# Kernel tuning notes

Hardware: AMD Instinct MI355X
Metric: run time of the kernel (lower is better)

Reference implementation:

```python
import jax, jax.numpy as jnp
import numpy as np
from jax import lax

B = 32        # true batch size (groups)
C_IN = 64     # per-sample input channels
C_OUT = 64    # per-sample output channels
H = W = 256
KH = KW = 3


def setup_inputs() -> dict:
    key = jax.random.key(0)
    kx, kk = jax.random.split(key)
    # x folds the batch into channels: [1, B*C_in, H, W]
    x = jax.random.normal(kx, (1, B * C_IN, H, W), dtype=jnp.float32)
    # per-sample kernels stacked along output-filter axis: [B*C_out, C_in, kH, kW]
    kernels = jax.random.normal(kk, (B * C_OUT, C_IN, KH, KW), dtype=jnp.float32)
    return {"x": x, "kernels": kernels, "batch_size": B}


def reference(x, kernels, batch_size):
    # F.conv2d(x, kernels, stride=1, padding='same', groups=batch_size)
    # Grouped conv with feature_group_count = batch_size (one group per sample).
    out = lax.conv_general_dilated(
        x,
        kernels,
        window_strides=(1, 1),
        padding="SAME",
        feature_group_count=batch_size,
        dimension_numbers=("NCHW", "OIHW", "NCHW"),
    )
    return out
```

## Files before the change

kernel.cpp:

```cpp
#include <hip/hip_runtime.h>
#include <hip/hip_bf16.h>


typedef __bf16 bf16x8 __attribute__((ext_vector_type(8)));
typedef float  f32x4  __attribute__((ext_vector_type(4)));

#define NB 32
#define NH 256
#define NW 256
#define TILE_H 4
#define TILE_W 64
#define XROWS 6
#define XCOLS 68
#define HWSZ ((size_t)NH * NW)

template<int P> struct IC { static constexpr int v = P; };

__device__ __forceinline__ void gload16(const float* g, float* lds) {
    __builtin_amdgcn_global_load_lds(
        (const __attribute__((address_space(1))) unsigned int*)g,
        (__attribute__((address_space(3))) unsigned int*)lds, 16, 0, 0);
}

__global__ void repack_weights_kernel(const float* __restrict__ wsrc,
                                      __bf16* __restrict__ pk) {
    int t = blockIdx.x * blockDim.x + threadIdx.x;
    if (t >= NB * 9 * 4 * 2 * 64) return;
    int lane = t & 63;
    int r = t >> 6;
    int kc = r & 1;  r >>= 1;
    int mt = r & 3;  r >>= 2;
    int tap = r % 9;
    int b   = r / 9;
    int co  = b * 64 + mt * 16 + (lane & 15);
    int ci0 = kc * 32 + (lane >> 4) * 8;
    bf16x8 v;
#pragma unroll
    for (int j = 0; j < 8; ++j) {
        v[j] = (__bf16)wsrc[(co * 64 + ci0 + j) * 9 + tap];
    }
    *reinterpret_cast<bf16x8*>(pk + (size_t)t * 8) = v;
}

__launch_bounds__(256)
__global__ void conv_mfma_kernel(const float* __restrict__ x,
                                 const __bf16* __restrict__ pk,
                                 float* __restrict__ out) {
    __shared__ __align__(16) __bf16 xs[XROWS * XCOLS * 32];
    __shared__ __align__(16) float  scratch[XROWS * 32 * 64];

    const int orig = blockIdx.x;
    const int wg   = (orig & 7) * 1024 + (orig >> 3);
    const int b    = wg >> 8;
    const int by   = (wg >> 2) & 63;
    const int bx   = wg & 3;
    const int h0   = by * TILE_H;
    const int w0   = bx * TILE_W;

    const int tid  = threadIdx.x;
    const int wid  = tid >> 6;
    const int lane = tid & 63;
    const int nl   = lane & 15;
    const int kgrp = lane >> 4;

    const __bf16* pkb = pk + (size_t)b * 9 * 4096;

    bf16x8 af[4][4];
    auto load_af = [&](int g) {
        const int tap = (g >= 9) ? g - 9 : g;
        const int kc  = (g >= 9) ? 1 : 0;
        const int sl  = g & 3;
#pragma unroll
        for (int mt = 0; mt < 4; ++mt)
            af[sl][mt] = *reinterpret_cast<const bf16x8*>(
                pkb + tap * 4096 + ((mt * 2 + kc) * 64 + lane) * 8);
    };

    f32x4 acc[4][4];
#pragma unroll
    for (int mt = 0; mt < 4; ++mt)
#pragma unroll
        for (int q = 0; q < 4; ++q)
            acc[mt][q] = (f32x4){0.f, 0.f, 0.f, 0.f};

    const int hside = tid & 1;
    const int hidx  = tid >> 1;
    const int hrr   = hidx % 6;
    const int hoo   = hidx / 6;
    const int hch   = hside ? 65 : 0;
    const int hwv   = hside ? (w0 + 64) : (w0 - 1);
    float hreg[8];
    bool  hz = false;

    auto issue_gload = [&](int kcv) {
#pragma unroll
        for (int m = 0; m < 12; ++m) {
            const int I  = wid * 12 + m;
            const int r  = I >> 3;
            const int cb = I & 7;
            const int hh = h0 - 1 + r;
            const int hc = min(max(hh, 0), NH - 1);
            const float* src = x
                + ((size_t)(b * 64 + kcv * 32 + cb * 4 + (lane >> 4)) * NH + hc) * NW
                + w0 + (lane & 15) * 4;
            gload16(src, scratch + (r * 32 + cb * 4) * 64);
        }
    };

    auto issue_halo = [&](int kcv) {
        if (tid < 48) {
            const int hh = h0 - 1 + hrr;
            hz = (hwv < 0) || (hwv > NW - 1) || (hh < 0) || (hh > NH - 1);
            const int wc2 = min(max(hwv, 0), NW - 1);
            const int hc2 = min(max(hh, 0), NH - 1);
            const float* s = x + ((size_t)(b * 64 + kcv * 32 + hoo * 8) * NH + hc2) * NW + wc2;
#pragma unroll
            for (int j = 0; j < 8; ++j) hreg[j] = s[j * HWSZ];
        }
    };

    auto cvt = [&]() {
#pragma unroll
        for (int rr = 0; rr < XROWS; ++rr) {
            const int hh = h0 - 1 + rr;
            const bool z = (hh < 0) || (hh > NH - 1);
            float v[8];
#pragma unroll
            for (int j = 0; j < 8; ++j)
                v[j] = scratch[(rr * 32 + wid * 8 + j) * 64 + lane];
            bf16x8 o8;
#pragma unroll
            for (int j = 0; j < 8; ++j) o8[j] = z ? (__bf16)0.f : (__bf16)v[j];
            const int c = lane + 1;
            *reinterpret_cast<bf16x8*>(
                xs + (rr * XCOLS + c) * 32 + ((wid ^ ((c >> 1) & 3)) * 8)) = o8;
        }
        if (tid < 48) {
            bf16x8 o8;
#pragma unroll
            for (int j = 0; j < 8; ++j) o8[j] = hz ? (__bf16)0.f : (__bf16)hreg[j];
            *reinterpret_cast<bf16x8*>(xs + (hrr * XCOLS + hch) * 32 + hoo * 8) = o8;
        }
    };

    auto comp = [&](auto parc, auto issc) {
        constexpr int PAR = decltype(parc)::v;
        constexpr int ISS = decltype(issc)::v;
#pragma unroll
        for (int tap = 0; tap < 9; ++tap) {
            const int g = PAR * 9 + tap;
            if (g + 2 < 18) load_af(g + 2);
            if constexpr (ISS) {
                if (tap == 3) { issue_gload(1); issue_halo(1); }
            }
            const int kh = tap / 3;
            const int kw = tap - kh * 3;
            const int rowbase = (wid + kh) * XCOLS;
            const int fs = g & 3;
#pragma unroll
            for (int q = 0; q < 4; ++q) {
                const int cc   = q * 16 + nl + kw;
                const int slot = (cc >> 1) & 3;
                bf16x8 bfv = *reinterpret_cast<const bf16x8*>(
                    xs + (rowbase + cc) * 32 + ((kgrp ^ slot) * 8));
#pragma unroll
                for (int mt = 0; mt < 4; ++mt)
                    acc[mt][q] = __builtin_amdgcn_mfma_f32_16x16x32_bf16(
                        af[fs][mt], bfv, acc[mt][q], 0, 0, 0);
            }
        }
    };

    load_af(0);
    load_af(1);
    issue_gload(0);
    issue_halo(0);
    __syncthreads();
    cvt();
    __syncthreads();
    comp(IC<0>{}, IC<1>{});
    __syncthreads();
    cvt();
    __syncthreads();
    comp(IC<1>{}, IC<0>{});

    const int mrow = kgrp * 4;
    const int h = h0 + wid;
#pragma unroll
    for (int mt = 0; mt < 4; ++mt) {
#pragma unroll
        for (int q = 0; q < 4; ++q) {
            const int ww = w0 + q * 16 + nl;
#pragma unroll
            for (int rg = 0; rg < 4; ++rg) {
                const int co = mt * 16 + mrow + rg;
                out[((size_t)(b * 64 + co) * NH + h) * NW + ww] = acc[mt][q][rg];
            }
        }
    }
}

extern "C" void kernel_launch(void* const* d_in, const int* in_sizes, int n_in,
                              void* d_out, int out_size, void* d_ws, size_t ws_size,
                              hipStream_t stream) {
    const float* x = (const float*)d_in[0];
    const float* w = (const float*)d_in[1];
    float* out = (float*)d_out;
    __bf16* pk = (__bf16*)d_ws;

    {
        int total = NB * 9 * 4 * 2 * 64;
        int blk = 256;
        int grid = (total + blk - 1) / blk;
        hipLaunchKernelGGL(repack_weights_kernel, dim3(grid), dim3(blk), 0, stream,
                           w, pk);
    }
    {
        dim3 grid(8192);
        hipLaunchKernelGGL(conv_mfma_kernel, grid, dim3(256), 0, stream,
                           x, pk, out);
    }
}
```

Measured before the change: 323.8 us.

## Split output channels across 8 waves and load halo via async LDS loads

Doubles the workgroup to 512 threads (8 waves), with each wave computing half of the 64 output channels for one row. All 9 taps of weights are preloaded per channel half instead of rotating 4 slots. The halo columns now go through global_load_lds into a small shared buffer rather than per-thread register loads, and the unused LDS padding shrinks from 68 to 66 columns. This raises the wave count per block to improve latency hiding, at the cost of more registers for the preloaded weights and duplicate B-fragment LDS reads across the two channel-halves.

```diff
diff --git a/kernel.cpp b/kernel.cpp
--- a/kernel.cpp
+++ b/kernel.cpp
@@ -11,7 +11,7 @@
 #define TILE_H 4
 #define TILE_W 64
 #define XROWS 6
-#define XCOLS 68
+#define XCOLS 66
 #define HWSZ ((size_t)NH * NW)
 
 template<int P> struct IC { static constexpr int v = P; };
@@ -20,6 +20,11 @@
     __builtin_amdgcn_global_load_lds(
         (const __attribute__((address_space(1))) unsigned int*)g,
         (__attribute__((address_space(3))) unsigned int*)lds, 16, 0, 0);
+}
+__device__ __forceinline__ void gload4(const float* g, float* lds) {
+    __builtin_amdgcn_global_load_lds(
+        (const __attribute__((address_space(1))) unsigned int*)g,
+        (__attribute__((address_space(3))) unsigned int*)lds, 4, 0, 0);
 }
 
 __global__ void repack_weights_kernel(const float* __restrict__ wsrc,
@@ -42,12 +47,13 @@
     *reinterpret_cast<bf16x8*>(pk + (size_t)t * 8) = v;
 }
 
-__launch_bounds__(256)
+__launch_bounds__(512, 4)
 __global__ void conv_mfma_kernel(const float* __restrict__ x,
                                  const __bf16* __restrict__ pk,
                                  float* __restrict__ out) {
     __shared__ __align__(16) __bf16 xs[XROWS * XCOLS * 32];
     __shared__ __align__(16) float  scratch[XROWS * 32 * 64];
+    __shared__ __align__(16) float  shalo[2 * XROWS * 32];
 
     const int orig = blockIdx.x;
     const int wg   = (orig & 7) * 1024 + (orig >> 3);
@@ -62,40 +68,33 @@
     const int lane = tid & 63;
     const int nl   = lane & 15;
     const int kgrp = lane >> 4;
+    const int rloc = wid >> 1;
+    const int ch   = wid & 1;
 
     const __bf16* pkb = pk + (size_t)b * 9 * 4096;
 
-    bf16x8 af[4][4];
-    auto load_af = [&](int g) {
-        const int tap = (g >= 9) ? g - 9 : g;
-        const int kc  = (g >= 9) ? 1 : 0;
-        const int sl  = g & 3;
-#pragma unroll
-        for (int mt = 0; mt < 4; ++mt)
-            af[sl][mt] = *reinterpret_cast<const bf16x8*>(
-                pkb + tap * 4096 + ((mt * 2 + kc) * 64 + lane) * 8);
-    };
-
-    f32x4 acc[4][4];
-#pragma unroll
-    for (int mt = 0; mt < 4; ++mt)
+    bf16x8 af[9][2];
+    auto load_af_bulk = [&](auto kcc) {
+        constexpr int KC = decltype(kcc)::v;
+#pragma unroll
+        for (int t = 0; t < 9; ++t)
+#pragma unroll
+            for (int mtl = 0; mtl < 2; ++mtl)
+                af[t][mtl] = *reinterpret_cast<const bf16x8*>(
+                    pkb + t * 4096 + (((ch * 2 + mtl) * 2 + KC) * 64 + lane) * 8);
+    };
+
+    f32x4 acc[2][4];
+#pragma unroll
+    for (int mtl = 0; mtl < 2; ++mtl)
 #pragma unroll
         for (int q = 0; q < 4; ++q)
-            acc[mt][q] = (f32x4){0.f, 0.f, 0.f, 0.f};
-
-    const int hside = tid & 1;
-    const int hidx  = tid >> 1;
-    const int hrr   = hidx % 6;
-    const int hoo   = hidx / 6;
-    const int hch   = hside ? 65 : 0;
-    const int hwv   = hside ? (w0 + 64) : (w0 - 1);
-    float hreg[8];
-    bool  hz = false;
+            acc[mtl][q] = (f32x4){0.f, 0.f, 0.f, 0.f};
 
     auto issue_gload = [&](int kcv) {
 #pragma unroll
-        for (int m = 0; m < 12; ++m) {
-            const int I  = wid * 12 + m;
+        for (int m = 0; m < 6; ++m) {
+            const int I  = wid * 6 + m;
             const int r  = I >> 3;
             const int cb = I & 7;
             const int hh = h0 - 1 + r;
@@ -105,58 +104,70 @@
                 + w0 + (lane & 15) * 4;
             gload16(src, scratch + (r * 32 + cb * 4) * 64);
         }
-    };
-
-    auto issue_halo = [&](int kcv) {
-        if (tid < 48) {
-            const int hh = h0 - 1 + hrr;
-            hz = (hwv < 0) || (hwv > NW - 1) || (hh < 0) || (hh > NH - 1);
-            const int wc2 = min(max(hwv, 0), NW - 1);
-            const int hc2 = min(max(hh, 0), NH - 1);
-            const float* s = x + ((size_t)(b * 64 + kcv * 32 + hoo * 8) * NH + hc2) * NW + wc2;
-#pragma unroll
-            for (int j = 0; j < 8; ++j) hreg[j] = s[j * HWSZ];
-        }
-    };
-
+        if (wid == 0) {
+#pragma unroll
+            for (int hI = 0; hI < 6; ++hI) {
+                const int side = hI & 1;
+                const int seg  = hI >> 1;
+                const int idx  = seg * 64 + lane;
+                const int r    = idx >> 5;
+                const int ci   = idx & 31;
+                const int wcol = min(max(w0 - 1 + side * 65, 0), NW - 1);
+                const int hh   = h0 - 1 + r;
+                const int hc   = min(max(hh, 0), NH - 1);
+                const float* src = x
+                    + ((size_t)(b * 64 + kcv * 32 + ci) * NH + hc) * NW + wcol;
+                gload4(src, shalo + side * 192 + seg * 64);
+            }
+        }
+    };
+
+    const int c    = lane;
+    const int oct  = wid & 3;
+    const int rset = wid >> 2;
     auto cvt = [&]() {
 #pragma unroll
-        for (int rr = 0; rr < XROWS; ++rr) {
+        for (int rr2 = 0; rr2 < 3; ++rr2) {
+            const int rr = rset * 3 + rr2;
             const int hh = h0 - 1 + rr;
             const bool z = (hh < 0) || (hh > NH - 1);
             float v[8];
 #pragma unroll
             for (int j = 0; j < 8; ++j)
-                v[j] = scratch[(rr * 32 + wid * 8 + j) * 64 + lane];
+                v[j] = scratch[(rr * 32 + oct * 8 + j) * 64 + c];
             bf16x8 o8;
 #pragma unroll
             for (int j = 0; j < 8; ++j) o8[j] = z ? (__bf16)0.f : (__bf16)v[j];
-            const int c = lane + 1;
+            const int cc = c + 1;
             *reinterpret_cast<bf16x8*>(
-                xs + (rr * XCOLS + c) * 32 + ((wid ^ ((c >> 1) & 3)) * 8)) = o8;
+                xs + (rr * XCOLS + cc) * 32 + ((oct ^ ((cc >> 1) & 3)) * 8)) = o8;
         }
         if (tid < 48) {
+            const int side = tid & 1;
+            const int q2   = tid >> 1;
+            const int rr   = q2 % 6;
+            const int ho   = q2 / 6;
+            const int hh   = h0 - 1 + rr;
+            const int wv   = w0 - 1 + side * 65;
+            const bool z = (hh < 0) || (hh > NH - 1) || (wv < 0) || (wv > NW - 1);
+            float v[8];
+#pragma unroll
+            for (int j = 0; j < 8; ++j)
+                v[j] = shalo[side * 192 + rr * 32 + ho * 8 + j];
             bf16x8 o8;
 #pragma unroll
-            for (int j = 0; j < 8; ++j) o8[j] = hz ? (__bf16)0.f : (__bf16)hreg[j];
-            *reinterpret_cast<bf16x8*>(xs + (hrr * XCOLS + hch) * 32 + hoo * 8) = o8;
-        }
-    };
-
-    auto comp = [&](auto parc, auto issc) {
-        constexpr int PAR = decltype(parc)::v;
-        constexpr int ISS = decltype(issc)::v;
+            for (int j = 0; j < 8; ++j) o8[j] = z ? (__bf16)0.f : (__bf16)v[j];
+            const int cc = side ? 65 : 0;
+            *reinterpret_cast<bf16x8*>(xs + (rr * XCOLS + cc) * 32 + ho * 8) = o8;
+        }
+    };
+
+    auto compute = [&]() {
 #pragma unroll
         for (int tap = 0; tap < 9; ++tap) {
-            const int g = PAR * 9 + tap;
-            if (g + 2 < 18) load_af(g + 2);
-            if constexpr (ISS) {
-                if (tap == 3) { issue_gload(1); issue_halo(1); }
-            }
             const int kh = tap / 3;
             const int kw = tap - kh * 3;
-            const int rowbase = (wid + kh) * XCOLS;
-            const int fs = g & 3;
+            const int rowbase = (rloc + kh) * XCOLS;
 #pragma unroll
             for (int q = 0; q < 4; ++q) {
                 const int cc   = q * 16 + nl + kw;
@@ -164,37 +175,37 @@
                 bf16x8 bfv = *reinterpret_cast<const bf16x8*>(
                     xs + (rowbase + cc) * 32 + ((kgrp ^ slot) * 8));
 #pragma unroll
-                for (int mt = 0; mt < 4; ++mt)
-                    acc[mt][q] = __builtin_amdgcn_mfma_f32_16x16x32_bf16(
-                        af[fs][mt], bfv, acc[mt][q], 0, 0, 0);
+                for (int mtl = 0; mtl < 2; ++mtl)
+                    acc[mtl][q] = __builtin_amdgcn_mfma_f32_16x16x32_bf16(
+                        af[tap][mtl], bfv, acc[mtl][q], 0, 0, 0);
             }
         }
     };
 
-    load_af(0);
-    load_af(1);
+    load_af_bulk(IC<0>{});
     issue_gload(0);
-    issue_halo(0);
     __syncthreads();
     cvt();
     __syncthreads();
-    comp(IC<0>{}, IC<1>{});
+    issue_gload(1);
+    compute();
     __syncthreads();
     cvt();
     __syncthreads();
-    comp(IC<1>{}, IC<0>{});
+    load_af_bulk(IC<1>{});
+    compute();
 
     const int mrow = kgrp * 4;
-    const int h = h0 + wid;
-#pragma unroll
-    for (int mt = 0; mt < 4; ++mt) {
+    const int h = h0 + rloc;
+#pragma unroll
+    for (int mtl = 0; mtl < 2; ++mtl) {
 #pragma unroll
         for (int q = 0; q < 4; ++q) {
             const int ww = w0 + q * 16 + nl;
 #pragma unroll
             for (int rg = 0; rg < 4; ++rg) {
-                const int co = mt * 16 + mrow + rg;
-                out[((size_t)(b * 64 + co) * NH + h) * NW + ww] = acc[mt][q][rg];
+                const int co = (ch * 2 + mtl) * 16 + mrow + rg;
+                out[((size_t)(b * 64 + co) * NH + h) * NW + ww] = acc[mtl][q][rg];
             }
         }
     }
@@ -217,7 +228,7 @@
     }
     {
         dim3 grid(8192);
-        hipLaunchKernelGGL(conv_mfma_kernel, grid, dim3(256), 0, stream,
+        hipLaunchKernelGGL(conv_mfma_kernel, grid, dim3(512), 0, stream,
                            x, pk, out);
     }
 }
```

Result: slower. 413.0 us (+27.5%).

## Double tile height to 8 rows with 512 threads and stage weights in LDS

Applied to the files above, without the earlier changes.

Each workgroup now computes 8 output rows, with 8 waves and 512 threads, instead of 4. This cuts the halo-row overhead from 6/4 to 10/8 and halves the grid. Weight fragments are now loaded into shared memory with global_load_lds, so each wave no longer keeps a 4-deep register pipeline of A fragments read from global memory. The second channel-chunk load is issued before compute rather than in the middle of it. In exchange, LDS per block grows considerably, which may reduce occupancy, and there is an extra LDS read per tap.

```diff
diff --git a/kernel.cpp b/kernel.cpp
--- a/kernel.cpp
+++ b/kernel.cpp
@@ -8,13 +8,11 @@
 #define NB 32
 #define NH 256
 #define NW 256
-#define TILE_H 4
+#define TILE_H 8
 #define TILE_W 64
-#define XROWS 6
-#define XCOLS 68
+#define XROWS 10
+#define XCOLS 66
 #define HWSZ ((size_t)NH * NW)
-
-template<int P> struct IC { static constexpr int v = P; };
 
 __device__ __forceinline__ void gload16(const float* g, float* lds) {
     __builtin_amdgcn_global_load_lds(
@@ -42,17 +40,18 @@
     *reinterpret_cast<bf16x8*>(pk + (size_t)t * 8) = v;
 }
 
-__launch_bounds__(256)
+__launch_bounds__(512)
 __global__ void conv_mfma_kernel(const float* __restrict__ x,
                                  const __bf16* __restrict__ pk,
                                  float* __restrict__ out) {
     __shared__ __align__(16) __bf16 xs[XROWS * XCOLS * 32];
+    __shared__ __align__(16) __bf16 afs[36 * 512];
     __shared__ __align__(16) float  scratch[XROWS * 32 * 64];
 
     const int orig = blockIdx.x;
-    const int wg   = (orig & 7) * 1024 + (orig >> 3);
-    const int b    = wg >> 8;
-    const int by   = (wg >> 2) & 63;
+    const int wg   = (orig & 7) * 512 + (orig >> 3);
+    const int b    = wg >> 7;
+    const int by   = (wg >> 2) & 31;
     const int bx   = wg & 3;
     const int h0   = by * TILE_H;
     const int w0   = bx * TILE_W;
@@ -63,39 +62,26 @@
     const int nl   = lane & 15;
     const int kgrp = lane >> 4;
 
-    const __bf16* pkb = pk + (size_t)b * 9 * 4096;
-
-    bf16x8 af[4][4];
-    auto load_af = [&](int g) {
-        const int tap = (g >= 9) ? g - 9 : g;
-        const int kc  = (g >= 9) ? 1 : 0;
-        const int sl  = g & 3;
-#pragma unroll
-        for (int mt = 0; mt < 4; ++mt)
-            af[sl][mt] = *reinterpret_cast<const bf16x8*>(
-                pkb + tap * 4096 + ((mt * 2 + kc) * 64 + lane) * 8);
-    };
-
-    f32x4 acc[4][4];
-#pragma unroll
-    for (int mt = 0; mt < 4; ++mt)
-#pragma unroll
-        for (int q = 0; q < 4; ++q)
-            acc[mt][q] = (f32x4){0.f, 0.f, 0.f, 0.f};
-
-    const int hside = tid & 1;
-    const int hidx  = tid >> 1;
-    const int hrr   = hidx % 6;
-    const int hoo   = hidx / 6;
-    const int hch   = hside ? 65 : 0;
-    const int hwv   = hside ? (w0 + 64) : (w0 - 1);
-    float hreg[8];
-    bool  hz = false;
-
-    auto issue_gload = [&](int kcv) {
-#pragma unroll
-        for (int m = 0; m < 12; ++m) {
-            const int I  = wid * 12 + m;
+    const char* pkb = (const char*)(pk + (size_t)b * 9 * 4096);
+
+    auto issue_af = [&](int kcv) {
+#pragma unroll
+        for (int i = 0; i < 5; ++i) {
+            const int f = wid + i * 8;
+            if (f < 36) {
+                const int tp = f >> 2;
+                const int mt = f & 3;
+                const float* src = (const float*)(pkb + tp * 8192
+                                                  + (mt * 2 + kcv) * 1024 + lane * 16);
+                gload16(src, (float*)((char*)afs + f * 1024));
+            }
+        }
+    };
+
+    auto issue_x = [&](int kcv) {
+#pragma unroll
+        for (int m = 0; m < 10; ++m) {
+            const int I  = wid * 10 + m;
             const int r  = I >> 3;
             const int cb = I & 7;
             const int hh = h0 - 1 + r;
@@ -107,56 +93,72 @@
         }
     };
 
+    const int hr    = tid >> 3;
+    const int hside = (tid >> 2) & 1;
+    const int hoct  = tid & 3;
+    const int hwv   = hside ? (w0 + 64) : (w0 - 1);
+    float hreg[8];
+    bool  hz = false;
+
     auto issue_halo = [&](int kcv) {
-        if (tid < 48) {
-            const int hh = h0 - 1 + hrr;
+        if (tid < 80) {
+            const int hh = h0 - 1 + hr;
             hz = (hwv < 0) || (hwv > NW - 1) || (hh < 0) || (hh > NH - 1);
             const int wc2 = min(max(hwv, 0), NW - 1);
             const int hc2 = min(max(hh, 0), NH - 1);
-            const float* s = x + ((size_t)(b * 64 + kcv * 32 + hoo * 8) * NH + hc2) * NW + wc2;
+            const float* s = x + ((size_t)(b * 64 + kcv * 32 + hoct * 8) * NH + hc2) * NW + wc2;
 #pragma unroll
             for (int j = 0; j < 8; ++j) hreg[j] = s[j * HWSZ];
         }
     };
 
+    const int c = lane;
     auto cvt = [&]() {
 #pragma unroll
-        for (int rr = 0; rr < XROWS; ++rr) {
-            const int hh = h0 - 1 + rr;
-            const bool z = (hh < 0) || (hh > NH - 1);
+        for (int k = 0; k < 5; ++k) {
+            const int p   = wid * 5 + k;
+            const int rr  = p >> 2;
+            const int oct = p & 3;
+            const int hh  = h0 - 1 + rr;
+            const bool z  = (hh < 0) || (hh > NH - 1);
             float v[8];
 #pragma unroll
             for (int j = 0; j < 8; ++j)
-                v[j] = scratch[(rr * 32 + wid * 8 + j) * 64 + lane];
+                v[j] = scratch[(rr * 32 + oct * 8 + j) * 64 + c];
             bf16x8 o8;
 #pragma unroll
             for (int j = 0; j < 8; ++j) o8[j] = z ? (__bf16)0.f : (__bf16)v[j];
-            const int c = lane + 1;
+            const int cc = c + 1;
             *reinterpret_cast<bf16x8*>(
-                xs + (rr * XCOLS + c) * 32 + ((wid ^ ((c >> 1) & 3)) * 8)) = o8;
-        }
-        if (tid < 48) {
+                xs + (rr * XCOLS + cc) * 32 + ((oct ^ ((cc >> 1) & 3)) * 8)) = o8;
+        }
+        if (tid < 80) {
             bf16x8 o8;
 #pragma unroll
             for (int j = 0; j < 8; ++j) o8[j] = hz ? (__bf16)0.f : (__bf16)hreg[j];
-            *reinterpret_cast<bf16x8*>(xs + (hrr * XCOLS + hch) * 32 + hoo * 8) = o8;
-        }
-    };
-
-    auto comp = [&](auto parc, auto issc) {
-        constexpr int PAR = decltype(parc)::v;
-        constexpr int ISS = decltype(issc)::v;
+            const int cc = hside ? 65 : 0;
+            *reinterpret_cast<bf16x8*>(xs + (hr * XCOLS + cc) * 32 + hoct * 8) = o8;
+        }
+    };
+
+    f32x4 acc[4][4];
+#pragma unroll
+    for (int mt = 0; mt < 4; ++mt)
+#pragma unroll
+        for (int q = 0; q < 4; ++q)
+            acc[mt][q] = (f32x4){0.f, 0.f, 0.f, 0.f};
+
+    auto compute = [&]() {
 #pragma unroll
         for (int tap = 0; tap < 9; ++tap) {
-            const int g = PAR * 9 + tap;
-            if (g + 2 < 18) load_af(g + 2);
-            if constexpr (ISS) {
-                if (tap == 3) { issue_gload(1); issue_halo(1); }
-            }
+            bf16x8 afr[4];
+#pragma unroll
+            for (int mt = 0; mt < 4; ++mt)
+                afr[mt] = *reinterpret_cast<const bf16x8*>(
+                    afs + (tap * 4 + mt) * 512 + lane * 8);
             const int kh = tap / 3;
             const int kw = tap - kh * 3;
             const int rowbase = (wid + kh) * XCOLS;
-            const int fs = g & 3;
 #pragma unroll
             for (int q = 0; q < 4; ++q) {
                 const int cc   = q * 16 + nl + kw;
@@ -166,23 +168,25 @@
 #pragma unroll
                 for (int mt = 0; mt < 4; ++mt)
                     acc[mt][q] = __builtin_amdgcn_mfma_f32_16x16x32_bf16(
-                        af[fs][mt], bfv, acc[mt][q], 0, 0, 0);
+                        afr[mt], bfv, acc[mt][q], 0, 0, 0);
             }
         }
     };
 
-    load_af(0);
-    load_af(1);
-    issue_gload(0);
+    issue_af(0);
+    issue_x(0);
     issue_halo(0);
     __syncthreads();
     cvt();
     __syncthreads();
-    comp(IC<0>{}, IC<1>{});
-    __syncthreads();
+    issue_x(1);
+    issue_halo(1);
+    compute();
+    __syncthreads();
+    issue_af(1);
     cvt();
     __syncthreads();
-    comp(IC<1>{}, IC<0>{});
+    compute();
 
     const int mrow = kgrp * 4;
     const int h = h0 + wid;
@@ -216,8 +220,8 @@
                            w, pk);
     }
     {
-        dim3 grid(8192);
-        hipLaunchKernelGGL(conv_mfma_kernel, grid, dim3(256), 0, stream,
+        dim3 grid(4096);
+        hipLaunchKernelGGL(conv_mfma_kernel, grid, dim3(512), 0, stream,
                            x, pk, out);
     }
 }
```

Result: faster. 304.6 us (-5.9%).
